# Kernel tuning notes

Hardware: AMD Instinct MI355X
Metric: run time of the kernel (lower is better)

The kernel has to match this reference:

```python
import jax, jax.numpy as jnp
import numpy as np

B, N, NPOINT, NSAMPLE = 8, 16384, 512, 64
RADIUS = 0.1
C_IN = 64
DIMS = [64, 64, 128]


def setup_inputs() -> dict:
    key = jax.random.key(0)
    ks = jax.random.split(key, 8)
    xyz = jax.random.uniform(ks[0], (B, N, 3), jnp.float32)          # points in unit cube
    features = jax.random.normal(ks[1], (B, C_IN, N), jnp.float32)   # (B, C, N) per GroupGatherByIndex
    dims = [3 + C_IN] + DIMS                                         # use_xyz_feature adds 3
    out = {"xyz": xyz, "features": features}
    for i in range(3):
        out[f"W{i+1}"] = jax.random.normal(ks[2 + i], (dims[i], dims[i + 1]), jnp.float32) / np.sqrt(dims[i])
        out[f"b{i+1}"] = jnp.zeros((dims[i + 1],), jnp.float32)
    return out


def furthest_point_sampling(xyz, npoint):
    # Iterative FPS starting at index 0 (matches CUDA kernel semantics).
    Bq, Nq, _ = xyz.shape
    barange = jnp.arange(Bq)

    def step(carry, _):
        dists, last = carry
        p = xyz[barange, last]                       # (B, 3)
        d = jnp.sum((xyz - p[:, None, :]) ** 2, -1)  # (B, N)
        dists = jnp.minimum(dists, d)
        nxt = jnp.argmax(dists, axis=1).astype(jnp.int32)
        return (dists, nxt), nxt

    init = (jnp.full((Bq, Nq), 1e10, xyz.dtype), jnp.zeros((Bq,), jnp.int32))
    _, idxs = jax.lax.scan(step, init, None, length=npoint - 1)
    return jnp.concatenate([jnp.zeros((Bq, 1), jnp.int32), idxs.T], axis=1)  # (B, npoint)


def ball_query(new_xyz, xyz, radius, nsample):
    # For each centroid, first nsample in-ball indices (ascending), padded with first hit.
    Nq = xyz.shape[1]
    d2 = jnp.sum((new_xyz[:, :, None, :] - xyz[:, None, :, :]) ** 2, -1)  # (B, npoint, N)
    cand = jnp.where(d2 < radius * radius, jnp.arange(Nq, dtype=jnp.int32), Nq)
    cand = jnp.sort(cand, axis=-1)[..., :nsample]                          # (B, npoint, nsample)
    first = jnp.where(cand[..., :1] == Nq, 0, cand[..., :1])
    return jnp.where(cand == Nq, first, cand)


def reference(xyz, features, W1, b1, W2, b2, W3, b3):
    fps_idx = furthest_point_sampling(xyz, NPOINT)                  # (B, npoint)
    new_xyz = jax.vmap(lambda p, i: p[i])(xyz, fps_idx)             # (B, npoint, 3)
    idx = ball_query(new_xyz, xyz, RADIUS, NSAMPLE)                 # (B, npoint, nsample)
    grouped_xyz = jax.vmap(lambda p, i: p[i])(xyz, idx)             # (B, npoint, nsample, 3)
    centered = grouped_xyz - new_xyz[:, :, None, :]                 # centroid subtract
    feats_n = jnp.transpose(features, (0, 2, 1))                    # (B, N, C)
    grouped_f = jax.vmap(lambda f, i: f[i])(feats_n, idx)           # (B, npoint, nsample, C)
    h = jnp.concatenate([centered, grouped_f], axis=-1)             # (B, npoint, nsample, 3+C)
    for W, b in ((W1, b1), (W2, b2), (W3, b3)):                     # pointwise 1x1-conv MLP + ReLU
        h = jax.nn.relu(h @ W + b)
    return jnp.max(h, axis=2)                                       # max-pool over nsample -> (B, npoint, C_out)
```

## Files before the change

### kernel.cpp

```cpp
#include <hip/hip_runtime.h>

#define NB 8
#define NPTS 16384
#define NPOINT 512
#define NSAMPLE 64
#define CIN 64

typedef float v2f __attribute__((ext_vector_type(2)));

__device__ __forceinline__ v2f pk_add(v2f a, v2f b) {
    v2f d;
    asm("v_pk_add_f32 %0, %1, %2" : "=v"(d) : "v"(a), "v"(b));
    return d;
}
__device__ __forceinline__ v2f pk_mul(v2f a, v2f b) {
    v2f d;
    asm("v_pk_mul_f32 %0, %1, %2" : "=v"(d) : "v"(a), "v"(b));
    return d;
}

template <int CTRL>
__device__ __forceinline__ float dpp_f(float x) {
    int xi = __builtin_bit_cast(int, x);
    int yi = __builtin_amdgcn_update_dpp(xi, xi, CTRL, 0xF, 0xF, false);
    return __builtin_bit_cast(float, yi);
}
template <int CTRL>
__device__ __forceinline__ int dpp_i(int x) {
    return __builtin_amdgcn_update_dpp(x, x, CTRL, 0xF, 0xF, false);
}

__device__ __forceinline__ float wave_max_f(float x) {
    x = fmaxf(x, dpp_f<0x111>(x));
    x = fmaxf(x, dpp_f<0x112>(x));
    x = fmaxf(x, dpp_f<0x114>(x));
    x = fmaxf(x, dpp_f<0x118>(x));
    x = fmaxf(x, dpp_f<0x142>(x));
    x = fmaxf(x, dpp_f<0x143>(x));
    return x;
}
__device__ __forceinline__ int wave_min_i(int x) {
    x = min(x, dpp_i<0x111>(x));
    x = min(x, dpp_i<0x112>(x));
    x = min(x, dpp_i<0x114>(x));
    x = min(x, dpp_i<0x118>(x));
    x = min(x, dpp_i<0x142>(x));
    x = min(x, dpp_i<0x143>(x));
    return x;
}

#define CMB(va, ia, vb, ib) { bool t_ = ((vb) > (va)) || (((vb) == (va)) && ((ib) < (ia))); \
                              if (t_) { (va) = (vb); (ia) = (ib); } }

__global__ __launch_bounds__(512, 1) void fps_transpose_kernel(
    const float* __restrict__ xyz, const float* __restrict__ feats,
    int* __restrict__ fps_idx, float* __restrict__ feats_t)
{
    __shared__ float t[64][65];
    __shared__ __align__(16) int s_pair[2][8][2];

    if (blockIdx.x >= NB) {
        int blk = blockIdx.x - NB;
        int b = blk & 7;
        int tile = blk >> 3;
        int n0 = tile * 64;
        int cc = threadIdx.x & 63, rr = threadIdx.x >> 6;
        const float* fb = feats + (size_t)b * CIN * NPTS;
        #pragma unroll
        for (int k = 0; k < 8; ++k) {
            int c = rr + k * 8;
            t[c][cc] = fb[(size_t)c * NPTS + n0 + cc];
        }
        __syncthreads();
        float* fo = feats_t + ((size_t)b * NPTS + n0) * CIN;
        #pragma unroll
        for (int k = 0; k < 8; ++k) {
            int n = rr + k * 8;
            fo[n * CIN + cc] = t[cc][n];
        }
        return;
    }

    const int b = blockIdx.x;
    const int tid = threadIdx.x;
    const int wv = tid >> 6, ln = tid & 63;
    const float* xb = xyz + (size_t)b * NPTS * 3;
    const int base = tid * 32;

    v2f px2[16], py2[16], pz2[16];
    float dd[32];
    {
        const float4* xb4 = (const float4*)(xb + (size_t)base * 3);
        #pragma unroll
        for (int q = 0; q < 8; ++q) {
            float4 f0 = xb4[3 * q + 0];
            float4 f1 = xb4[3 * q + 1];
            float4 f2 = xb4[3 * q + 2];
            px2[2 * q + 0] = (v2f){f0.x, f0.w};
            py2[2 * q + 0] = (v2f){f0.y, f1.x};
            pz2[2 * q + 0] = (v2f){f0.z, f1.y};
            px2[2 * q + 1] = (v2f){f1.z, f2.y};
            py2[2 * q + 1] = (v2f){f1.w, f2.z};
            pz2[2 * q + 1] = (v2f){f2.x, f2.w};
        }
        #pragma unroll
        for (int k = 0; k < 32; ++k) dd[k] = 1e10f;
    }
    if (tid == 0) fps_idx[b * NPOINT] = 0;
    float cx = xb[0], cy = xb[1], cz = xb[2];
    __syncthreads();

    for (int j = 1; j < NPOINT; ++j) {
        const int p = j & 1;
        v2f ncx = (v2f){-cx, -cx};
        v2f ncy = (v2f){-cy, -cy};
        v2f ncz = (v2f){-cz, -cz};
        float bm = -1.0f;
        #pragma unroll
        for (int k = 0; k < 16; ++k) {
            v2f dx = pk_add(px2[k], ncx);
            v2f dy = pk_add(py2[k], ncy);
            v2f dz = pk_add(pz2[k], ncz);
            v2f sx = pk_mul(dx, dx);
            v2f sy = pk_mul(dy, dy);
            v2f sz = pk_mul(dz, dz);
            v2f s1 = pk_add(sx, sy);
            v2f d2 = pk_add(s1, sz);
            float n0 = fminf(dd[2 * k + 0], d2.x);
            float n1 = fminf(dd[2 * k + 1], d2.y);
            dd[2 * k + 0] = n0;
            dd[2 * k + 1] = n1;
            bm = fmaxf(fmaxf(bm, n0), n1);
        }
        float wm = wave_max_f(bm);
        float wmax = __builtin_bit_cast(float,
            __builtin_amdgcn_readlane(__builtin_bit_cast(int, wm), 63));
        int mi = 0x7fffffff;
        #pragma unroll
        for (int k = 31; k >= 0; --k)
            mi = (dd[k] == wmax) ? (base + k) : mi;
        int rm = wave_min_i(mi);
        int wave_mi = __builtin_amdgcn_readlane(rm, 63);
        if (ln == 0) {
            s_pair[p][wv][0] = __builtin_bit_cast(int, wmax);
            s_pair[p][wv][1] = wave_mi;
        }
        __syncthreads();
        int4 q0 = *(const int4*)&s_pair[p][0][0];
        int4 q1 = *(const int4*)&s_pair[p][2][0];
        int4 q2 = *(const int4*)&s_pair[p][4][0];
        int4 q3 = *(const int4*)&s_pair[p][6][0];
        float v0 = __builtin_bit_cast(float, q0.x); int i0 = q0.y;
        float v1 = __builtin_bit_cast(float, q0.z); int i1 = q0.w;
        float v2 = __builtin_bit_cast(float, q1.x); int i2 = q1.y;
        float v3 = __builtin_bit_cast(float, q1.z); int i3 = q1.w;
        float v4 = __builtin_bit_cast(float, q2.x); int i4 = q2.y;
        float v5 = __builtin_bit_cast(float, q2.z); int i5 = q2.w;
        float v6 = __builtin_bit_cast(float, q3.x); int i6 = q3.y;
        float v7 = __builtin_bit_cast(float, q3.z); int i7 = q3.w;
        CMB(v0, i0, v1, i1); CMB(v2, i2, v3, i3);
        CMB(v4, i4, v5, i5); CMB(v6, i6, v7, i7);
        CMB(v0, i0, v2, i2); CMB(v4, i4, v6, i6);
        CMB(v0, i0, v4, i4);
        int ch = __builtin_amdgcn_readfirstlane(i0);
        const float* cp = xb + 3 * ch;
        cx = cp[0]; cy = cp[1]; cz = cp[2];
        if (tid == 0) fps_idx[b * NPOINT + j] = ch;
    }
}

__global__ __launch_bounds__(64) void ball_kernel(
    const float* __restrict__ xyz, const int* __restrict__ fps_idx, int* __restrict__ ball_idx)
{
    const float R2 = (float)(0.1 * 0.1);
    int blk = blockIdx.x;
    int b = blk & 7, j = blk >> 3;
    int lane = threadIdx.x;
    int cent = b * NPOINT + j;
    const float* xb = xyz + (size_t)b * NPTS * 3;
    int cidx = fps_idx[cent];
    float cx = xb[3 * cidx + 0];
    float cy = xb[3 * cidx + 1];
    float cz = xb[3 * cidx + 2];

    __shared__ int slots[64];
    int cnt = 0;
    for (int base = 0; base < NPTS; base += 64) {
        int i = base + lane;
        float dx = __fsub_rn(xb[3 * i + 0], cx);
        float dy = __fsub_rn(xb[3 * i + 1], cy);
        float dz = __fsub_rn(xb[3 * i + 2], cz);
        float d2 = __fadd_rn(__fadd_rn(__fmul_rn(dx, dx), __fmul_rn(dy, dy)), __fmul_rn(dz, dz));
        bool inb = d2 < R2;
        unsigned long long m = __ballot(inb);
        int pre = (int)__popcll(m & ((1ull << lane) - 1ull));
        int slot = cnt + pre;
        if (inb && slot < NSAMPLE) slots[slot] = i;
        cnt += (int)__popcll(m);
        if (cnt >= NSAMPLE) break;
    }
    __syncthreads();
    int first = (cnt > 0) ? slots[0] : 0;
    int v = (lane < cnt) ? slots[lane] : first;
    ball_idx[(size_t)cent * NSAMPLE + lane] = v;
}

__global__ __launch_bounds__(64) void mlp_kernel(
    const float* __restrict__ xyz, const float* __restrict__ feats_t,
    const int* __restrict__ fps_idx, const int* __restrict__ ball_idx,
    const float* __restrict__ W1, const float* __restrict__ b1,
    const float* __restrict__ W2, const float* __restrict__ b2,
    const float* __restrict__ W3, const float* __restrict__ b3,
    float* __restrict__ out)
{
    int blk = blockIdx.x;
    int b = blk & 7, j = blk >> 3;
    int s = threadIdx.x;
    int cent = b * NPOINT + j;

    __shared__ float X[64][68];

    int i = ball_idx[(size_t)cent * NSAMPLE + s];
    int cidx = fps_idx[cent];
    const float* cp = xyz + ((size_t)b * NPTS + cidx) * 3;
    float cx = cp[0], cy = cp[1], cz = cp[2];
    const float* pp = xyz + ((size_t)b * NPTS + i) * 3;
    X[s][64] = pp[0] - cx;
    X[s][65] = pp[1] - cy;
    X[s][66] = pp[2] - cz;
    const float4* fr = (const float4*)(feats_t + ((size_t)b * NPTS + i) * CIN);
    #pragma unroll
    for (int q = 0; q < 16; ++q) *(float4*)&X[s][q * 4] = fr[q];

    float acc[64];
    #pragma unroll
    for (int o = 0; o < 64; ++o) acc[o] = b1[o];
    for (int c = 0; c < 67; ++c) {
        float xc = X[s][c];
        const float* w = W1 + ((c < 64) ? (c + 3) : (c - 64)) * 64;
        #pragma unroll
        for (int o = 0; o < 64; ++o) acc[o] = fmaf(xc, w[o], acc[o]);
    }
    #pragma unroll
    for (int o = 0; o < 64; ++o) X[s][o] = fmaxf(acc[o], 0.0f);

    #pragma unroll
    for (int o = 0; o < 64; ++o) acc[o] = b2[o];
    for (int c = 0; c < 64; ++c) {
        float xc = X[s][c];
        const float* w = W2 + c * 64;
        #pragma unroll
        for (int o = 0; o < 64; ++o) acc[o] = fmaf(xc, w[o], acc[o]);
    }
    #pragma unroll
    for (int o = 0; o < 64; ++o) X[s][o] = fmaxf(acc[o], 0.0f);

    float h3[128];
    #pragma unroll
    for (int o = 0; o < 128; ++o) h3[o] = b3[o];
    for (int c = 0; c < 64; ++c) {
        float xc = X[s][c];
        const float* w = W3 + c * 128;
        #pragma unroll
        for (int o = 0; o < 128; ++o) h3[o] = fmaf(xc, w[o], h3[o]);
    }

    #pragma unroll
    for (int o = 0; o < 128; ++o) {
        float v = fmaxf(h3[o], 0.0f);
        #pragma unroll
        for (int off = 1; off < 64; off <<= 1) v = fmaxf(v, __shfl_xor(v, off));
        h3[o] = v;
    }
    if (s == 0) {
        float* op = out + (size_t)cent * 128;
        #pragma unroll
        for (int o = 0; o < 128; o += 4) {
            float4 v = make_float4(h3[o], h3[o + 1], h3[o + 2], h3[o + 3]);
            *(float4*)&op[o] = v;
        }
    }
}

extern "C" void kernel_launch(void* const* d_in, const int* in_sizes, int n_in,
                              void* d_out, int out_size, void* d_ws, size_t ws_size,
                              hipStream_t stream) {
    const float* xyz   = (const float*)d_in[0];
    const float* feats = (const float*)d_in[1];
    const float* W1 = (const float*)d_in[2];
    const float* b1 = (const float*)d_in[3];
    const float* W2 = (const float*)d_in[4];
    const float* b2 = (const float*)d_in[5];
    const float* W3 = (const float*)d_in[6];
    const float* b3 = (const float*)d_in[7];
    float* out = (float*)d_out;

    char* ws = (char*)d_ws;
    int*   fps_idx  = (int*)ws;
    int*   ball_idx = (int*)(ws + 16384);
    float* feats_t  = (float*)(ws + 16384 + 1048576);

    fps_transpose_kernel<<<NB + NB * (NPTS / 64), 512, 0, stream>>>(xyz, feats, fps_idx, feats_t);
    ball_kernel<<<NB * NPOINT, 64, 0, stream>>>(xyz, fps_idx, ball_idx);
    mlp_kernel<<<NB * NPOINT, 64, 0, stream>>>(xyz, feats_t, fps_idx, ball_idx,
                                               W1, b1, W2, b2, W3, b3, out);
}
```

Baseline: 1.244 ms.

## Use compiler vector ops in FPS, relax occupancy hint, transpose MLP LDS layout

```diff
diff --git a/kernel.cpp b/kernel.cpp
--- a/kernel.cpp
+++ b/kernel.cpp
@@ -7,17 +7,6 @@
 #define CIN 64
 
 typedef float v2f __attribute__((ext_vector_type(2)));
-
-__device__ __forceinline__ v2f pk_add(v2f a, v2f b) {
-    v2f d;
-    asm("v_pk_add_f32 %0, %1, %2" : "=v"(d) : "v"(a), "v"(b));
-    return d;
-}
-__device__ __forceinline__ v2f pk_mul(v2f a, v2f b) {
-    v2f d;
-    asm("v_pk_mul_f32 %0, %1, %2" : "=v"(d) : "v"(a), "v"(b));
-    return d;
-}
 
 template <int CTRL>
 __device__ __forceinline__ float dpp_f(float x) {
@@ -52,7 +41,8 @@
 #define CMB(va, ia, vb, ib) { bool t_ = ((vb) > (va)) || (((vb) == (va)) && ((ib) < (ia))); \
                               if (t_) { (va) = (vb); (ia) = (ib); } }
 
-__global__ __launch_bounds__(512, 1) void fps_transpose_kernel(
+__global__ __launch_bounds__(512) __attribute__((amdgpu_waves_per_eu(2, 2)))
+void fps_transpose_kernel(
     const float* __restrict__ xyz, const float* __restrict__ feats,
     int* __restrict__ fps_idx, float* __restrict__ feats_t)
 {
@@ -87,8 +77,7 @@
     const float* xb = xyz + (size_t)b * NPTS * 3;
     const int base = tid * 32;
 
-    v2f px2[16], py2[16], pz2[16];
-    float dd[32];
+    v2f px2[16], py2[16], pz2[16], dd2[16];
     {
         const float4* xb4 = (const float4*)(xb + (size_t)base * 3);
         #pragma unroll
@@ -104,13 +93,14 @@
             pz2[2 * q + 1] = (v2f){f2.x, f2.w};
         }
         #pragma unroll
-        for (int k = 0; k < 32; ++k) dd[k] = 1e10f;
+        for (int k = 0; k < 16; ++k) dd2[k] = (v2f){1e10f, 1e10f};
     }
     if (tid == 0) fps_idx[b * NPOINT] = 0;
     float cx = xb[0], cy = xb[1], cz = xb[2];
     __syncthreads();
 
     for (int j = 1; j < NPOINT; ++j) {
+        #pragma clang fp contract(off)
         const int p = j & 1;
         v2f ncx = (v2f){-cx, -cx};
         v2f ncy = (v2f){-cy, -cy};
@@ -118,27 +108,25 @@
         float bm = -1.0f;
         #pragma unroll
         for (int k = 0; k < 16; ++k) {
-            v2f dx = pk_add(px2[k], ncx);
-            v2f dy = pk_add(py2[k], ncy);
-            v2f dz = pk_add(pz2[k], ncz);
-            v2f sx = pk_mul(dx, dx);
-            v2f sy = pk_mul(dy, dy);
-            v2f sz = pk_mul(dz, dz);
-            v2f s1 = pk_add(sx, sy);
-            v2f d2 = pk_add(s1, sz);
-            float n0 = fminf(dd[2 * k + 0], d2.x);
-            float n1 = fminf(dd[2 * k + 1], d2.y);
-            dd[2 * k + 0] = n0;
-            dd[2 * k + 1] = n1;
-            bm = fmaxf(fmaxf(bm, n0), n1);
+            v2f dx = px2[k] + ncx;
+            v2f dy = py2[k] + ncy;
+            v2f dz = pz2[k] + ncz;
+            v2f s1 = dx * dx + dy * dy;
+            v2f d2 = s1 + dz * dz;
+            v2f nd = __builtin_elementwise_min(dd2[k], d2);
+            dd2[k] = nd;
+            bm = fmaxf(bm, fmaxf(nd.x, nd.y));
         }
         float wm = wave_max_f(bm);
         float wmax = __builtin_bit_cast(float,
             __builtin_amdgcn_readlane(__builtin_bit_cast(int, wm), 63));
-        int mi = 0x7fffffff;
-        #pragma unroll
-        for (int k = 31; k >= 0; --k)
-            mi = (dd[k] == wmax) ? (base + k) : mi;
+        int mk = 64;
+        #pragma unroll
+        for (int k = 15; k >= 0; --k) {
+            mk = (dd2[k].y == wmax) ? (2 * k + 1) : mk;
+            mk = (dd2[k].x == wmax) ? (2 * k)     : mk;
+        }
+        int mi = (mk == 64) ? 0x7fffffff : (base + mk);
         int rm = wave_min_i(mi);
         int wave_mi = __builtin_amdgcn_readlane(rm, 63);
         if (ln == 0) {
@@ -218,48 +206,54 @@
     int s = threadIdx.x;
     int cent = b * NPOINT + j;
 
-    __shared__ float X[64][68];
+    __shared__ float X[67][64];
 
     int i = ball_idx[(size_t)cent * NSAMPLE + s];
     int cidx = fps_idx[cent];
     const float* cp = xyz + ((size_t)b * NPTS + cidx) * 3;
     float cx = cp[0], cy = cp[1], cz = cp[2];
     const float* pp = xyz + ((size_t)b * NPTS + i) * 3;
-    X[s][64] = pp[0] - cx;
-    X[s][65] = pp[1] - cy;
-    X[s][66] = pp[2] - cz;
+    X[64][s] = pp[0] - cx;
+    X[65][s] = pp[1] - cy;
+    X[66][s] = pp[2] - cz;
     const float4* fr = (const float4*)(feats_t + ((size_t)b * NPTS + i) * CIN);
     #pragma unroll
-    for (int q = 0; q < 16; ++q) *(float4*)&X[s][q * 4] = fr[q];
+    for (int q = 0; q < 16; ++q) {
+        float4 f = fr[q];
+        X[q * 4 + 0][s] = f.x;
+        X[q * 4 + 1][s] = f.y;
+        X[q * 4 + 2][s] = f.z;
+        X[q * 4 + 3][s] = f.w;
+    }
 
     float acc[64];
     #pragma unroll
     for (int o = 0; o < 64; ++o) acc[o] = b1[o];
     for (int c = 0; c < 67; ++c) {
-        float xc = X[s][c];
+        float xc = X[c][s];
         const float* w = W1 + ((c < 64) ? (c + 3) : (c - 64)) * 64;
         #pragma unroll
         for (int o = 0; o < 64; ++o) acc[o] = fmaf(xc, w[o], acc[o]);
     }
     #pragma unroll
-    for (int o = 0; o < 64; ++o) X[s][o] = fmaxf(acc[o], 0.0f);
+    for (int o = 0; o < 64; ++o) X[o][s] = fmaxf(acc[o], 0.0f);
 
     #pragma unroll
     for (int o = 0; o < 64; ++o) acc[o] = b2[o];
     for (int c = 0; c < 64; ++c) {
-        float xc = X[s][c];
+        float xc = X[c][s];
         const float* w = W2 + c * 64;
         #pragma unroll
         for (int o = 0; o < 64; ++o) acc[o] = fmaf(xc, w[o], acc[o]);
     }
     #pragma unroll
-    for (int o = 0; o < 64; ++o) X[s][o] = fmaxf(acc[o], 0.0f);
+    for (int o = 0; o < 64; ++o) X[o][s] = fmaxf(acc[o], 0.0f);
 
     float h3[128];
     #pragma unroll
     for (int o = 0; o < 128; ++o) h3[o] = b3[o];
     for (int c = 0; c < 64; ++c) {
-        float xc = X[s][c];
+        float xc = X[c][s];
         const float* w = W3 + c * 128;
         #pragma unroll
         for (int o = 0; o < 128; ++o) h3[o] = fmaf(xc, w[o], h3[o]);
```

Measured after the change: 1.190 ms. 4.4% less time.
